# Optimization experiments

Measured on AMD Instinct MI355X. Metric: run time of the kernel, lower is better.

Reference implementation:

```python
import jax, jax.numpy as jnp
import numpy as np

B, T, D = 2048, 200, 64
H1, H2 = 80, 40
NEG_INF = -4294967295.0  # -(2**32) + 1 as in original


def setup_inputs() -> dict:
    key0 = jax.random.key(0)
    ks = jax.random.split(key0, 10)
    din_dim = 4 * D
    inp = {
        "query": jax.random.normal(ks[0], (B, D), dtype=jnp.float32),
        "key": jax.random.normal(ks[1], (B, T, D), dtype=jnp.float32),
        "mask": jax.random.randint(ks[2], (B,), 1, T + 1, dtype=jnp.int32),
        # MLP params (Dense 4D->80->40->1, use_bias=True)
        "W1": jax.random.normal(ks[3], (din_dim, H1), dtype=jnp.float32) / np.sqrt(din_dim),
        "b1": jnp.zeros((H1,), dtype=jnp.float32),
        "W2": jax.random.normal(ks[4], (H1, H2), dtype=jnp.float32) / np.sqrt(H1),
        "b2": jnp.zeros((H2,), dtype=jnp.float32),
        "W3": jax.random.normal(ks[5], (H2, 1), dtype=jnp.float32) / np.sqrt(H2),
        "b3": jnp.zeros((1,), dtype=jnp.float32),
    }
    return inp


def reference(query, key, mask, W1, b1, W2, b2, W3, b3):
    b, t, d = key.shape
    q = query[:, None, :]                      # [B,1,D]
    q_tile = jnp.broadcast_to(q, (b, t, d))    # [B,T,D]
    din_all = jnp.concatenate([q_tile, key, q_tile - key, q_tile * key], axis=-1)  # [B,T,4D]
    h = jax.nn.sigmoid(jnp.einsum("btf,fh->bth", din_all, W1) + b1)
    h = jax.nn.sigmoid(jnp.einsum("bth,hg->btg", h, W2) + b2)
    score = (jnp.einsum("btg,go->bto", h, W3) + b3)[..., 0]  # [B,T]
    key_mask = jnp.arange(t)[None, :] < mask[:, None]        # [B,T]
    score = jnp.where(key_mask, score, NEG_INF)
    score = score / jnp.asarray(d, score.dtype) ** 0.5
    attn = jax.nn.softmax(score, axis=-1)                    # [B,T]
    out = jnp.einsum("bt,btd->bd", attn, key)                # [B,D] (squeezed)
    return out
```

## Files before the change

kernel.cpp:

```cpp
#include <hip/hip_runtime.h>
#include <math.h>

#define B_  2048
#define T_  200
#define D_  64
#define H1_ 80
#define H2_ 40

#define WSTR 104
#define NLOG2E (-1.4426950408889634f)
#define LOG2E  (1.4426950408889634f)

#define WS_A    0
#define WS_C    10240
#define WS_W2T  20480
#define WS_ACT  30464

typedef __bf16 bf16x8 __attribute__((ext_vector_type(8)));
typedef float  f32x4  __attribute__((ext_vector_type(4)));

__device__ __forceinline__ float sigmoid2_(float y) {
    return __builtin_amdgcn_rcpf(1.0f + __builtin_amdgcn_exp2f(y));
}
__device__ __forceinline__ unsigned pk2_(float a, float b) {
    __bf16 x = (__bf16)a, y = (__bf16)b;
    unsigned short ux = __builtin_bit_cast(unsigned short, x);
    unsigned short uy = __builtin_bit_cast(unsigned short, y);
    return (unsigned)ux | ((unsigned)uy << 16);
}

__global__ __launch_bounds__(256)
void prep_kernel(const float* __restrict__ W1, const float* __restrict__ W2,
                 void* __restrict__ ws)
{
    __bf16* A    = (__bf16*)((char*)ws + WS_A);
    __bf16* C    = (__bf16*)((char*)ws + WS_C);
    __bf16* W2Tp = (__bf16*)((char*)ws + WS_W2T);
    float*  acT  = (float*)((char*)ws + WS_ACT);
    const int e0 = blockIdx.x * 256 + threadIdx.x;

    for (int e = e0; e < H1_ * D_; e += 2048) {
        int h = e >> 6, f = e & 63;
        float wb = W1[(64  + f) * H1_ + h];
        float wc = W1[(128 + f) * H1_ + h];
        float wd = W1[(192 + f) * H1_ + h];
        float wa = W1[f * H1_ + h];
        A[e]   = (__bf16)(NLOG2E * (wb - wc));
        C[e]   = (__bf16)(NLOG2E * wd);
        acT[e] = wa + wc;
    }
    for (int e = e0; e < 48 * WSTR; e += 2048) {
        int g = e / WSTR, h = e - g * WSTR;
        W2Tp[e] = (g < H2_ && h < H1_) ? (__bf16)(NLOG2E * W2[h * H2_ + g]) : (__bf16)0.0f;
    }
}

__global__ __launch_bounds__(256, 2)
void attn_din20(const float* __restrict__ query,
                const float* __restrict__ key,
                const int*   __restrict__ mask,
                const float* __restrict__ b1,
                const float* __restrict__ b2,
                const float* __restrict__ W3,
                const float* __restrict__ b3,
                const void*  __restrict__ ws,
                float* __restrict__ out)
{
    __shared__ __align__(16) float s_q[4][D_];
    __shared__ float s_base[4][H1_];
    __shared__ float s_part[4][D_];

    const int tid  = threadIdx.x;
    const int lane = tid & 63;
    const int w    = tid >> 6;
    const int c16  = lane & 15;
    const int g16  = lane >> 4;
    const int b    = blockIdx.x * 4 + w;

    const int   mv     = mask[b];
    const int   npairs = (mv + 31) >> 5;
    const float b3s    = b3[0] * 0.125f * LOG2E;
    const float* kb = key + (size_t)b * T_ * D_;

    const __bf16* wsA   = (const __bf16*)((const char*)ws + WS_A);
    const __bf16* wsC   = (const __bf16*)((const char*)ws + WS_C);
    const __bf16* wsW2T = (const __bf16*)((const char*)ws + WS_W2T);
    const float*  wsacT = (const float*) ((const char*)ws + WS_ACT);

    float qv = query[b * D_ + lane];
    float4 uA0, uA1, uA2, uA3, uB0, uB1, uB2, uB3;
    {
        const float* krA = kb + (size_t)c16 * D_ + g16 * 8;
        const float* krB = kb + (size_t)(16 + c16) * D_ + g16 * 8;
        uA0 = *(const float4*)(krA);      uA1 = *(const float4*)(krA + 4);
        uA2 = *(const float4*)(krA + 32); uA3 = *(const float4*)(krA + 36);
        uB0 = *(const float4*)(krB);      uB1 = *(const float4*)(krB + 4);
        uB2 = *(const float4*)(krB + 32); uB3 = *(const float4*)(krB + 36);
    }
    s_q[w][lane] = qv;

    bf16x8 bw[3][3];
    #pragma unroll
    for (int nt = 0; nt < 3; ++nt)
        #pragma unroll
        for (int ks = 0; ks < 3; ++ks)
            bw[nt][ks] = *(const bf16x8*)&wsW2T[(nt * 16 + c16) * WSTR + ks * 32 + g16 * 8];

    float b2c[3][4], w3c[3][4];
    #pragma unroll
    for (int nt = 0; nt < 3; ++nt)
        #pragma unroll
        for (int r = 0; r < 4; ++r) {
            int g = nt * 16 + g16 * 4 + r;
            b2c[nt][r] = (g < H2_) ? b2[g] * NLOG2E : 0.0f;
            w3c[nt][r] = (g < H2_) ? W3[g] * 0.125f * LOG2E : 0.0f;
        }

    {
        float a0 = b1[lane], a1 = 0.0f, a2 = 0.0f, a3 = 0.0f;
        const f32x4* row = (const f32x4*)&wsacT[lane * D_];
        #pragma unroll
        for (int f4 = 0; f4 < 16; ++f4) {
            f32x4 v  = row[f4];
            f32x4 q4 = *(const f32x4*)&s_q[w][f4 * 4];
            a0 = fmaf(q4[0], v[0], a0);
            a1 = fmaf(q4[1], v[1], a1);
            a2 = fmaf(q4[2], v[2], a2);
            a3 = fmaf(q4[3], v[3], a3);
        }
        s_base[w][lane] = (a0 + a1) + (a2 + a3);
    }
    if (lane < 16) {
        int h = 64 + lane;
        float a0 = b1[h], a1 = 0.0f, a2 = 0.0f, a3 = 0.0f;
        const f32x4* row = (const f32x4*)&wsacT[h * D_];
        #pragma unroll
        for (int f4 = 0; f4 < 16; ++f4) {
            f32x4 v  = row[f4];
            f32x4 q4 = *(const f32x4*)&s_q[w][f4 * 4];
            a0 = fmaf(q4[0], v[0], a0);
            a1 = fmaf(q4[1], v[1], a1);
            a2 = fmaf(q4[2], v[2], a2);
            a3 = fmaf(q4[3], v[3], a3);
        }
        s_base[w][h] = (a0 + a1) + (a2 + a3);
    }

    bf16x8 bv[5][2];
    #pragma unroll
    for (int mt = 0; mt < 5; ++mt)
        #pragma unroll
        for (int ks = 0; ks < 2; ++ks) {
            int off = (mt * 16 + c16) * D_ + ks * 32 + g16 * 8;
            bf16x8 a8 = *(const bf16x8*)&wsA[off];
            bf16x8 c8 = *(const bf16x8*)&wsC[off];
            f32x4 q0 = *(const f32x4*)&s_q[w][ks * 32 + g16 * 8];
            f32x4 q1 = *(const f32x4*)&s_q[w][ks * 32 + g16 * 8 + 4];
            bf16x8 v8;
            v8[0] = (__bf16)((float)a8[0] + q0[0] * (float)c8[0]);
            v8[1] = (__bf16)((float)a8[1] + q0[1] * (float)c8[1]);
            v8[2] = (__bf16)((float)a8[2] + q0[2] * (float)c8[2]);
            v8[3] = (__bf16)((float)a8[3] + q0[3] * (float)c8[3]);
            v8[4] = (__bf16)((float)a8[4] + q1[0] * (float)c8[4]);
            v8[5] = (__bf16)((float)a8[5] + q1[1] * (float)c8[5]);
            v8[6] = (__bf16)((float)a8[6] + q1[2] * (float)c8[6]);
            v8[7] = (__bf16)((float)a8[7] + q1[3] * (float)c8[7]);
            bv[mt][ks] = v8;
        }

    float base_c[5][4];
    #pragma unroll
    for (int mt = 0; mt < 5; ++mt)
        #pragma unroll
        for (int r = 0; r < 4; ++r)
            base_c[mt][r] = s_base[w][16 * mt + g16 * 4 + r] * NLOG2E;

    const int  L0 = ((g16 & 1) << 5) + c16;
    const int  L1 = L0 + 16;
    const bool hi = (g16 >= 2);

    float o00,o01,o02,o03,o04,o05,o06,o07,o08,o09,o10,o11,o12,o13,o14,o15;
    o00=o01=o02=o03=o04=o05=o06=o07=o08=o09=o10=o11=o12=o13=o14=o15=0.0f;
    float l_run = 0.0f;

    for (int pp = 0; pp < npairs; ++pp) {
        bf16x8 afA0, afA1, afB0, afB1;
        afA0[0]=(__bf16)uA0.x; afA0[1]=(__bf16)uA0.y; afA0[2]=(__bf16)uA0.z; afA0[3]=(__bf16)uA0.w;
        afA0[4]=(__bf16)uA1.x; afA0[5]=(__bf16)uA1.y; afA0[6]=(__bf16)uA1.z; afA0[7]=(__bf16)uA1.w;
        afA1[0]=(__bf16)uA2.x; afA1[1]=(__bf16)uA2.y; afA1[2]=(__bf16)uA2.z; afA1[3]=(__bf16)uA2.w;
        afA1[4]=(__bf16)uA3.x; afA1[5]=(__bf16)uA3.y; afA1[6]=(__bf16)uA3.z; afA1[7]=(__bf16)uA3.w;
        afB0[0]=(__bf16)uB0.x; afB0[1]=(__bf16)uB0.y; afB0[2]=(__bf16)uB0.z; afB0[3]=(__bf16)uB0.w;
        afB0[4]=(__bf16)uB1.x; afB0[5]=(__bf16)uB1.y; afB0[6]=(__bf16)uB1.z; afB0[7]=(__bf16)uB1.w;
        afB1[0]=(__bf16)uB2.x; afB1[1]=(__bf16)uB2.y; afB1[2]=(__bf16)uB2.z; afB1[3]=(__bf16)uB2.w;
        afB1[4]=(__bf16)uB3.x; afB1[5]=(__bf16)uB3.y; afB1[6]=(__bf16)uB3.z; afB1[7]=(__bf16)uB3.w;

        if (pp + 1 < npairs) {
            int trA = (pp + 1) * 32 + c16;
            int trB = trA + 16;
            const float* krA = kb + (size_t)((trA < T_) ? trA : (T_ - 1)) * D_ + g16 * 8;
            const float* krB = kb + (size_t)((trB < T_) ? trB : (T_ - 1)) * D_ + g16 * 8;
            uA0 = *(const float4*)(krA);      uA1 = *(const float4*)(krA + 4);
            uA2 = *(const float4*)(krA + 32); uA3 = *(const float4*)(krA + 36);
            uB0 = *(const float4*)(krB);      uB1 = *(const float4*)(krB + 4);
            uB2 = *(const float4*)(krB + 32); uB3 = *(const float4*)(krB + 36);
        }

        unsigned pkA[5][2], pkB[5][2];
        __builtin_amdgcn_s_setprio(1);
        #pragma unroll
        for (int mt = 0; mt < 5; ++mt) {
            f32x4 cA = { base_c[mt][0], base_c[mt][1], base_c[mt][2], base_c[mt][3] };
            cA = __builtin_amdgcn_mfma_f32_16x16x32_bf16(bv[mt][0], afA0, cA, 0, 0, 0);
            cA = __builtin_amdgcn_mfma_f32_16x16x32_bf16(bv[mt][1], afA1, cA, 0, 0, 0);
            f32x4 cB = { base_c[mt][0], base_c[mt][1], base_c[mt][2], base_c[mt][3] };
            cB = __builtin_amdgcn_mfma_f32_16x16x32_bf16(bv[mt][0], afB0, cB, 0, 0, 0);
            cB = __builtin_amdgcn_mfma_f32_16x16x32_bf16(bv[mt][1], afB1, cB, 0, 0, 0);
            pkA[mt][0] = pk2_(sigmoid2_(cA[0]), sigmoid2_(cA[1]));
            pkA[mt][1] = pk2_(sigmoid2_(cA[2]), sigmoid2_(cA[3]));
            pkB[mt][0] = pk2_(sigmoid2_(cB[0]), sigmoid2_(cB[1]));
            pkB[mt][1] = pk2_(sigmoid2_(cB[2]), sigmoid2_(cB[3]));
        }
        __builtin_amdgcn_s_setprio(0);

        float sA, sB;
        #pragma unroll
        for (int sub = 0; sub < 2; ++sub) {
            unsigned w00,w01,w02,w03, w10,w11,w12,w13, w20,w21,w22,w23;
            {
                #define PKX(m,i) (sub ? pkB[m][i] : pkA[m][i])
                unsigned a,bq;
                a = __shfl(PKX(0,0), L0); bq = __shfl(PKX(1,0), L0); w00 = hi ? bq : a;
                a = __shfl(PKX(0,1), L0); bq = __shfl(PKX(1,1), L0); w01 = hi ? bq : a;
                a = __shfl(PKX(0,0), L1); bq = __shfl(PKX(1,0), L1); w02 = hi ? bq : a;
                a = __shfl(PKX(0,1), L1); bq = __shfl(PKX(1,1), L1); w03 = hi ? bq : a;
                a = __shfl(PKX(2,0), L0); bq = __shfl(PKX(3,0), L0); w10 = hi ? bq : a;
                a = __shfl(PKX(2,1), L0); bq = __shfl(PKX(3,1), L0); w11 = hi ? bq : a;
                a = __shfl(PKX(2,0), L1); bq = __shfl(PKX(3,0), L1); w12 = hi ? bq : a;
                a = __shfl(PKX(2,1), L1); bq = __shfl(PKX(3,1), L1); w13 = hi ? bq : a;
                a = __shfl(PKX(4,0), L0);                            w20 = hi ? 0u : a;
                a = __shfl(PKX(4,1), L0);                            w21 = hi ? 0u : a;
                a = __shfl(PKX(4,0), L1);                            w22 = hi ? 0u : a;
                a = __shfl(PKX(4,1), L1);                            w23 = hi ? 0u : a;
                #undef PKX
            }
            union { unsigned u[4]; bf16x8 v; } cv0, cv1, cv2;
            cv0.u[0]=w00; cv0.u[1]=w01; cv0.u[2]=w02; cv0.u[3]=w03;
            cv1.u[0]=w10; cv1.u[1]=w11; cv1.u[2]=w12; cv1.u[3]=w13;
            cv2.u[0]=w20; cv2.u[1]=w21; cv2.u[2]=w22; cv2.u[3]=w23;

            float p0 = 0.0f, p1 = 0.0f, p2 = 0.0f, p3 = 0.0f;
            __builtin_amdgcn_s_setprio(1);
            #pragma unroll
            for (int nt2 = 0; nt2 < 3; ++nt2) {
                f32x4 c = { b2c[nt2][0], b2c[nt2][1], b2c[nt2][2], b2c[nt2][3] };
                c = __builtin_amdgcn_mfma_f32_16x16x32_bf16(bw[nt2][0], cv0.v, c, 0, 0, 0);
                c = __builtin_amdgcn_mfma_f32_16x16x32_bf16(bw[nt2][1], cv1.v, c, 0, 0, 0);
                c = __builtin_amdgcn_mfma_f32_16x16x32_bf16(bw[nt2][2], cv2.v, c, 0, 0, 0);
                p0 = fmaf(sigmoid2_(c[0]), w3c[nt2][0], p0);
                p1 = fmaf(sigmoid2_(c[1]), w3c[nt2][1], p1);
                p2 = fmaf(sigmoid2_(c[2]), w3c[nt2][2], p2);
                p3 = fmaf(sigmoid2_(c[3]), w3c[nt2][3], p3);
            }
            __builtin_amdgcn_s_setprio(0);
            float partial = (p0 + p1) + (p2 + p3);
            partial += __shfl_xor(partial, 16);
            partial += __shfl_xor(partial, 32);
            float sc = partial + b3s;
            if (sub == 0) sA = sc; else sB = sc;
        }

        const int tb = pp * 32;
        float pA = (tb + c16 < mv)      ? __builtin_amdgcn_exp2f(sA) : 0.0f;
        float pB = (tb + 16 + c16 < mv) ? __builtin_amdgcn_exp2f(sB) : 0.0f;
        l_run += pA + pB;

        o00 = fmaf(pB, (float)afB0[0], fmaf(pA, (float)afA0[0], o00));
        o01 = fmaf(pB, (float)afB0[1], fmaf(pA, (float)afA0[1], o01));
        o02 = fmaf(pB, (float)afB0[2], fmaf(pA, (float)afA0[2], o02));
        o03 = fmaf(pB, (float)afB0[3], fmaf(pA, (float)afA0[3], o03));
        o04 = fmaf(pB, (float)afB0[4], fmaf(pA, (float)afA0[4], o04));
        o05 = fmaf(pB, (float)afB0[5], fmaf(pA, (float)afA0[5], o05));
        o06 = fmaf(pB, (float)afB0[6], fmaf(pA, (float)afA0[6], o06));
        o07 = fmaf(pB, (float)afB0[7], fmaf(pA, (float)afA0[7], o07));
        o08 = fmaf(pB, (float)afB1[0], fmaf(pA, (float)afA1[0], o08));
        o09 = fmaf(pB, (float)afB1[1], fmaf(pA, (float)afA1[1], o09));
        o10 = fmaf(pB, (float)afB1[2], fmaf(pA, (float)afA1[2], o10));
        o11 = fmaf(pB, (float)afB1[3], fmaf(pA, (float)afA1[3], o11));
        o12 = fmaf(pB, (float)afB1[4], fmaf(pA, (float)afA1[4], o12));
        o13 = fmaf(pB, (float)afB1[5], fmaf(pA, (float)afA1[5], o13));
        o14 = fmaf(pB, (float)afB1[6], fmaf(pA, (float)afA1[6], o14));
        o15 = fmaf(pB, (float)afB1[7], fmaf(pA, (float)afA1[7], o15));
    }

    #define ORED(X) X += __shfl_xor(X,1); X += __shfl_xor(X,2); X += __shfl_xor(X,4); X += __shfl_xor(X,8);
    ORED(o00) ORED(o01) ORED(o02) ORED(o03) ORED(o04) ORED(o05) ORED(o06) ORED(o07)
    ORED(o08) ORED(o09) ORED(o10) ORED(o11) ORED(o12) ORED(o13) ORED(o14) ORED(o15)
    ORED(l_run)
    #undef ORED
    float inv_total = __builtin_amdgcn_rcpf(l_run);
    if (c16 == 0) {
        float* sp = &s_part[w][0];
        sp[g16 * 8 + 0] = o00;  sp[g16 * 8 + 1] = o01;
        sp[g16 * 8 + 2] = o02;  sp[g16 * 8 + 3] = o03;
        sp[g16 * 8 + 4] = o04;  sp[g16 * 8 + 5] = o05;
        sp[g16 * 8 + 6] = o06;  sp[g16 * 8 + 7] = o07;
        sp[32 + g16 * 8 + 0] = o08;  sp[32 + g16 * 8 + 1] = o09;
        sp[32 + g16 * 8 + 2] = o10;  sp[32 + g16 * 8 + 3] = o11;
        sp[32 + g16 * 8 + 4] = o12;  sp[32 + g16 * 8 + 5] = o13;
        sp[32 + g16 * 8 + 6] = o14;  sp[32 + g16 * 8 + 7] = o15;
    }
    asm volatile("s_waitcnt lgkmcnt(0)" ::: "memory");
    out[b * D_ + lane] = s_part[w][lane] * inv_total;
}

extern "C" void kernel_launch(void* const* d_in, const int* in_sizes, int n_in,
                              void* d_out, int out_size, void* d_ws, size_t ws_size,
                              hipStream_t stream)
{
    const float* query = (const float*)d_in[0];
    const float* key   = (const float*)d_in[1];
    const int*   mask  = (const int*)  d_in[2];
    const float* W1    = (const float*)d_in[3];
    const float* b1    = (const float*)d_in[4];
    const float* W2    = (const float*)d_in[5];
    const float* b2    = (const float*)d_in[6];
    const float* W3    = (const float*)d_in[7];
    const float* b3    = (const float*)d_in[8];
    float* out = (float*)d_out;

    prep_kernel<<<8, 256, 0, stream>>>(W1, W2, d_ws);
    attn_din20<<<512, 256, 0, stream>>>(query, key, mask, b1, b2, W3, b3, d_ws, out);
}
```

Before: 41.64 us.

## Split each batch row's sequence across two waves and combine partials

Each block now handles two batch rows instead of four, with two waves per row that take alternating 32-token chunks. Partial weighted sums and softmax denominators go to shared memory and are combined after a block barrier. This roughly halves the serial loop length per wave and doubles the grid to improve latency hiding and load balance across variable mask lengths. In exchange, the per-row setup (base projection, weight fragments) is duplicated across both waves and a __syncthreads is added. The combine assumes a fixed softmax offset rather than a running max, as the existing code already does.

```diff
diff --git a/kernel.cpp b/kernel.cpp
--- a/kernel.cpp
+++ b/kernel.cpp
@@ -56,7 +56,7 @@
 }
 
 __global__ __launch_bounds__(256, 2)
-void attn_din20(const float* __restrict__ query,
+void attn_din21(const float* __restrict__ query,
                 const float* __restrict__ key,
                 const int*   __restrict__ mask,
                 const float* __restrict__ b1,
@@ -66,16 +66,19 @@
                 const void*  __restrict__ ws,
                 float* __restrict__ out)
 {
-    __shared__ __align__(16) float s_q[4][D_];
-    __shared__ float s_base[4][H1_];
+    __shared__ __align__(16) float s_q[2][D_];
+    __shared__ float s_base[2][H1_];
     __shared__ float s_part[4][D_];
+    __shared__ float s_l[4];
 
     const int tid  = threadIdx.x;
     const int lane = tid & 63;
     const int w    = tid >> 6;
+    const int bs   = w >> 1;
+    const int wp   = w & 1;
     const int c16  = lane & 15;
     const int g16  = lane >> 4;
-    const int b    = blockIdx.x * 4 + w;
+    const int b    = blockIdx.x * 2 + bs;
 
     const int   mv     = mask[b];
     const int   npairs = (mv + 31) >> 5;
@@ -90,14 +93,14 @@
     float qv = query[b * D_ + lane];
     float4 uA0, uA1, uA2, uA3, uB0, uB1, uB2, uB3;
     {
-        const float* krA = kb + (size_t)c16 * D_ + g16 * 8;
-        const float* krB = kb + (size_t)(16 + c16) * D_ + g16 * 8;
+        const float* krA = kb + (size_t)(wp * 32 + c16) * D_ + g16 * 8;
+        const float* krB = kb + (size_t)(wp * 32 + 16 + c16) * D_ + g16 * 8;
         uA0 = *(const float4*)(krA);      uA1 = *(const float4*)(krA + 4);
         uA2 = *(const float4*)(krA + 32); uA3 = *(const float4*)(krA + 36);
         uB0 = *(const float4*)(krB);      uB1 = *(const float4*)(krB + 4);
         uB2 = *(const float4*)(krB + 32); uB3 = *(const float4*)(krB + 36);
     }
-    s_q[w][lane] = qv;
+    s_q[bs][lane] = qv;
 
     bf16x8 bw[3][3];
     #pragma unroll
@@ -122,13 +125,13 @@
         #pragma unroll
         for (int f4 = 0; f4 < 16; ++f4) {
             f32x4 v  = row[f4];
-            f32x4 q4 = *(const f32x4*)&s_q[w][f4 * 4];
+            f32x4 q4 = *(const f32x4*)&s_q[bs][f4 * 4];
             a0 = fmaf(q4[0], v[0], a0);
             a1 = fmaf(q4[1], v[1], a1);
             a2 = fmaf(q4[2], v[2], a2);
             a3 = fmaf(q4[3], v[3], a3);
         }
-        s_base[w][lane] = (a0 + a1) + (a2 + a3);
+        s_base[bs][lane] = (a0 + a1) + (a2 + a3);
     }
     if (lane < 16) {
         int h = 64 + lane;
@@ -137,13 +140,13 @@
         #pragma unroll
         for (int f4 = 0; f4 < 16; ++f4) {
             f32x4 v  = row[f4];
-            f32x4 q4 = *(const f32x4*)&s_q[w][f4 * 4];
+            f32x4 q4 = *(const f32x4*)&s_q[bs][f4 * 4];
             a0 = fmaf(q4[0], v[0], a0);
             a1 = fmaf(q4[1], v[1], a1);
             a2 = fmaf(q4[2], v[2], a2);
             a3 = fmaf(q4[3], v[3], a3);
         }
-        s_base[w][h] = (a0 + a1) + (a2 + a3);
+        s_base[bs][h] = (a0 + a1) + (a2 + a3);
     }
 
     bf16x8 bv[5][2];
@@ -154,8 +157,8 @@
             int off = (mt * 16 + c16) * D_ + ks * 32 + g16 * 8;
             bf16x8 a8 = *(const bf16x8*)&wsA[off];
             bf16x8 c8 = *(const bf16x8*)&wsC[off];
-            f32x4 q0 = *(const f32x4*)&s_q[w][ks * 32 + g16 * 8];
-            f32x4 q1 = *(const f32x4*)&s_q[w][ks * 32 + g16 * 8 + 4];
+            f32x4 q0 = *(const f32x4*)&s_q[bs][ks * 32 + g16 * 8];
+            f32x4 q1 = *(const f32x4*)&s_q[bs][ks * 32 + g16 * 8 + 4];
             bf16x8 v8;
             v8[0] = (__bf16)((float)a8[0] + q0[0] * (float)c8[0]);
             v8[1] = (__bf16)((float)a8[1] + q0[1] * (float)c8[1]);
@@ -173,7 +176,7 @@
     for (int mt = 0; mt < 5; ++mt)
         #pragma unroll
         for (int r = 0; r < 4; ++r)
-            base_c[mt][r] = s_base[w][16 * mt + g16 * 4 + r] * NLOG2E;
+            base_c[mt][r] = s_base[bs][16 * mt + g16 * 4 + r] * NLOG2E;
 
     const int  L0 = ((g16 & 1) << 5) + c16;
     const int  L1 = L0 + 16;
@@ -183,7 +186,7 @@
     o00=o01=o02=o03=o04=o05=o06=o07=o08=o09=o10=o11=o12=o13=o14=o15=0.0f;
     float l_run = 0.0f;
 
-    for (int pp = 0; pp < npairs; ++pp) {
+    for (int pp = wp; pp < npairs; pp += 2) {
         bf16x8 afA0, afA1, afB0, afB1;
         afA0[0]=(__bf16)uA0.x; afA0[1]=(__bf16)uA0.y; afA0[2]=(__bf16)uA0.z; afA0[3]=(__bf16)uA0.w;
         afA0[4]=(__bf16)uA1.x; afA0[5]=(__bf16)uA1.y; afA0[6]=(__bf16)uA1.z; afA0[7]=(__bf16)uA1.w;
@@ -194,8 +197,8 @@
         afB1[0]=(__bf16)uB2.x; afB1[1]=(__bf16)uB2.y; afB1[2]=(__bf16)uB2.z; afB1[3]=(__bf16)uB2.w;
         afB1[4]=(__bf16)uB3.x; afB1[5]=(__bf16)uB3.y; afB1[6]=(__bf16)uB3.z; afB1[7]=(__bf16)uB3.w;
 
-        if (pp + 1 < npairs) {
-            int trA = (pp + 1) * 32 + c16;
+        if (pp + 2 < npairs) {
+            int trA = (pp + 2) * 32 + c16;
             int trB = trA + 16;
             const float* krA = kb + (size_t)((trA < T_) ? trA : (T_ - 1)) * D_ + g16 * 8;
             const float* krB = kb + (size_t)((trB < T_) ? trB : (T_ - 1)) * D_ + g16 * 8;
@@ -297,7 +300,6 @@
     ORED(o08) ORED(o09) ORED(o10) ORED(o11) ORED(o12) ORED(o13) ORED(o14) ORED(o15)
     ORED(l_run)
     #undef ORED
-    float inv_total = __builtin_amdgcn_rcpf(l_run);
     if (c16 == 0) {
         float* sp = &s_part[w][0];
         sp[g16 * 8 + 0] = o00;  sp[g16 * 8 + 1] = o01;
@@ -309,8 +311,17 @@
         sp[32 + g16 * 8 + 4] = o12;  sp[32 + g16 * 8 + 5] = o13;
         sp[32 + g16 * 8 + 6] = o14;  sp[32 + g16 * 8 + 7] = o15;
     }
-    asm volatile("s_waitcnt lgkmcnt(0)" ::: "memory");
-    out[b * D_ + lane] = s_part[w][lane] * inv_total;
+    if (lane == 0) s_l[w] = l_run;
+    __syncthreads();
+
+    if ((tid & 127) < D_) {
+        int k  = tid >> 7;
+        int d  = tid & 63;
+        int bo = blockIdx.x * 2 + k;
+        float ot = s_part[2 * k][d] + s_part[2 * k + 1][d];
+        float lt = s_l[2 * k] + s_l[2 * k + 1];
+        out[bo * D_ + d] = ot * __builtin_amdgcn_rcpf(lt);
+    }
 }
 
 extern "C" void kernel_launch(void* const* d_in, const int* in_sizes, int n_in,
@@ -329,5 +340,5 @@
     float* out = (float*)d_out;
 
     prep_kernel<<<8, 256, 0, stream>>>(W1, W2, d_ws);
-    attn_din20<<<512, 256, 0, stream>>>(query, key, mask, b1, b2, W3, b3, d_ws, out);
-}
+    attn_din21<<<B_ / 2, 256, 0, stream>>>(query, key, mask, b1, b2, W3, b3, d_ws, out);
+}
```

Result: slower. 51.10 us (+22.7%).

## Sort batches by mask length and pair long/short rows per 8-wave block

Applied to the files above, without the earlier changes.

Adds a single-block counting-sort kernel that orders batch rows by mask length (descending) and builds a permutation that puts four long rows and four short rows in each block. The attention kernel grows to 512 threads (8 waves, one row each) and reads its row index from the permutation. This balances the variable-length work across blocks and waves to cut tail imbalance. It costs an extra serial launch and one indirect index load per wave.

```diff
diff --git a/kernel.cpp b/kernel.cpp
--- a/kernel.cpp
+++ b/kernel.cpp
@@ -15,6 +15,7 @@
 #define WS_C    10240
 #define WS_W2T  20480
 #define WS_ACT  30464
+#define WS_PERM 51200
 
 typedef __bf16 bf16x8 __attribute__((ext_vector_type(8)));
 typedef float  f32x4  __attribute__((ext_vector_type(4)));
@@ -55,8 +56,40 @@
     }
 }
 
-__global__ __launch_bounds__(256, 2)
-void attn_din20(const float* __restrict__ query,
+__global__ __launch_bounds__(256)
+void sort_kernel(const int* __restrict__ mask, void* __restrict__ ws)
+{
+    int* perm = (int*)((char*)ws + WS_PERM);
+    __shared__ int hist[201];
+    __shared__ int pfx[201];
+    __shared__ int S[B_];
+    const int tid = threadIdx.x;
+
+    for (int i = tid; i <= 200; i += 256) hist[i] = 0;
+    __syncthreads();
+    for (int b = tid; b < B_; b += 256) atomicAdd(&hist[mask[b]], 1);
+    __syncthreads();
+    if (tid == 0) {
+        int acc = 0;
+        for (int v = 200; v >= 1; --v) { pfx[v] = acc; acc += hist[v]; }
+    }
+    __syncthreads();
+    for (int i = tid; i <= 200; i += 256) hist[i] = 0;
+    __syncthreads();
+    for (int b = tid; b < B_; b += 256) {
+        int v = mask[b];
+        int pos = pfx[v] + atomicAdd(&hist[v], 1);
+        S[pos] = b;
+    }
+    __syncthreads();
+    for (int i = tid; i < B_; i += 256) {
+        int blk = i >> 3, w = i & 7;
+        perm[i] = (w < 4) ? S[blk * 4 + w] : S[2047 - blk * 4 - (w - 4)];
+    }
+}
+
+__global__ __launch_bounds__(512, 2)
+void attn_din22(const float* __restrict__ query,
                 const float* __restrict__ key,
                 const int*   __restrict__ mask,
                 const float* __restrict__ b1,
@@ -66,16 +99,18 @@
                 const void*  __restrict__ ws,
                 float* __restrict__ out)
 {
-    __shared__ __align__(16) float s_q[4][D_];
-    __shared__ float s_base[4][H1_];
-    __shared__ float s_part[4][D_];
+    __shared__ __align__(16) float s_q[8][D_];
+    __shared__ float s_base[8][H1_];
+    __shared__ float s_part[8][D_];
 
     const int tid  = threadIdx.x;
     const int lane = tid & 63;
     const int w    = tid >> 6;
     const int c16  = lane & 15;
     const int g16  = lane >> 4;
-    const int b    = blockIdx.x * 4 + w;
+
+    const int* perm = (const int*)((const char*)ws + WS_PERM);
+    const int b = perm[blockIdx.x * 8 + w];
 
     const int   mv     = mask[b];
     const int   npairs = (mv + 31) >> 5;
@@ -329,5 +364,6 @@
     float* out = (float*)d_out;
 
     prep_kernel<<<8, 256, 0, stream>>>(W1, W2, d_ws);
-    attn_din20<<<512, 256, 0, stream>>>(query, key, mask, b1, b2, W3, b3, d_ws, out);
-}
+    sort_kernel<<<1, 256, 0, stream>>>(mask, d_ws);
+    attn_din22<<<B_ / 8, 512, 0, stream>>>(query, key, mask, b1, b2, W3, b3, d_ws, out);
+}
```

Measured after the change: 42.72 us. +2.6%, slower.
